# Kernel tuning notes

Hardware: AMD Instinct MI355X
Metric: run time of the kernel (lower is better)

## Reference

```python
import jax, jax.numpy as jnp
import numpy as np

B, N = 4, 8192
NPOINT, NSAMPLE = 2048, 16
IN_PLANES, OUT_PLANES = 64, 128
EPS = 1e-5


def farthest_point_sample(xyz, npoint):
    # xyz: (B, N, 3) -> (B, npoint) int32 indices. Deterministic start at index 0
    # (torch version uses a random start; fixed start keeps the reference reproducible).
    Bb, Nn, _ = xyz.shape

    def step(carry, _):
        distance, farthest = carry                                   # (B,N), (B,)
        centroid = jnp.take_along_axis(xyz, farthest[:, None, None], axis=1)  # (B,1,3)
        dist = jnp.sum((xyz - centroid) ** 2, axis=-1)               # (B,N)
        distance = jnp.minimum(distance, dist)
        new_farthest = jnp.argmax(distance, axis=-1).astype(jnp.int32)
        return (distance, new_farthest), farthest

    init = (jnp.full((Bb, Nn), 1e10, xyz.dtype), jnp.zeros((Bb,), jnp.int32))
    _, cents = jax.lax.scan(step, init, None, length=npoint)         # (npoint, B)
    return cents.T                                                   # (B, npoint)


def setup_inputs() -> dict:
    key = jax.random.key(0)
    k1, k2, k3 = jax.random.split(key, 3)
    px = jax.random.normal(k1, (B, N, IN_PLANES), jnp.float32)
    xyz = jax.random.uniform(k2, (B, N, 3), jnp.float32)
    # Linear(3+in_planes -> out_planes), stored as (in, out)
    W = jax.random.normal(k3, (3 + IN_PLANES, OUT_PLANES), jnp.float32) * 0.1
    b = jnp.zeros((OUT_PLANES,), jnp.float32)
    gamma = jnp.ones((OUT_PLANES,), jnp.float32)
    beta = jnp.zeros((OUT_PLANES,), jnp.float32)
    return {"px": px, "xyz": xyz, "W": W, "b": b, "gamma": gamma, "beta": beta}


def reference(px, xyz, W, b, gamma, beta):
    Bb, Nn, C = px.shape
    cent_idx = farthest_point_sample(xyz, NPOINT)                    # (B, npoint)
    new_xyz = jnp.take_along_axis(xyz, cent_idx[:, :, None], axis=1) # (B, npoint, 3)

    # squared pairwise distances, clamped at 0 (matches square_distance)
    dists = (jnp.sum(new_xyz ** 2, -1)[..., None]
             + jnp.sum(xyz ** 2, -1)[:, None, :]
             - 2.0 * jnp.einsum('bmc,bnc->bmn', new_xyz, xyz))       # (B, npoint, N)
    dists = jnp.maximum(dists, 0.0)

    # KNN: top_k on negated dists == argsort()[:, :, :nsample] up to ties
    _, idx = jax.lax.top_k(-dists, NSAMPLE)                          # (B, npoint, nsample)

    gather = jax.vmap(lambda pts, i: pts[i])                         # per-batch fancy gather
    grouped_xyz = gather(xyz, idx)                                   # (B, npoint, nsample, 3)
    grouped_px = gather(px, idx)                                     # (B, npoint, nsample, C)
    grouped_xyz_norm = grouped_xyz - new_xyz[:, :, None, :]
    grouped = jnp.concatenate([grouped_px, grouped_xyz_norm], axis=-1)

    # Linear -> BatchNorm1d (training-mode batch stats, biased var) -> ReLU
    h = grouped.reshape(-1, C + 3) @ W + b                           # (B*npoint*nsample, out)
    mu = jnp.mean(h, axis=0)
    var = jnp.var(h, axis=0)
    h = (h - mu) / jnp.sqrt(var + EPS) * gamma + beta
    h = jax.nn.relu(h)

    new_px = jnp.max(h.reshape(Bb, NPOINT, NSAMPLE, -1), axis=2)     # (B, npoint, out)
    return new_px, new_xyz
```

## Files before the change

kernel.cpp:

```cpp
#include <hip/hip_runtime.h>
#include <math.h>

#define Bc 4
#define Nc 8192
#define NPOINTc 2048
#define NSAMPLEc 16
#define CINc 64
#define COUTc 128
#define FDIMc 67
#define NBUCK 128
#define EPSc 1e-5f

typedef unsigned long long u64;

__global__ void sq_norm_kernel(const float* __restrict__ xyz, float* __restrict__ sn) {
    int i = blockIdx.x * blockDim.x + threadIdx.x;
    if (i < Bc * Nc) {
        float x = xyz[i * 3], y = xyz[i * 3 + 1], z = xyz[i * 3 + 2];
        sn[i] = __fadd_rn(__fadd_rn(__fmul_rn(x, x), __fmul_rn(y, y)), __fmul_rn(z, z));
    }
}

template <int CTRL>
__device__ __forceinline__ float dpp_maxf(float x) {
    const float o = __int_as_float(__builtin_amdgcn_update_dpp(
        __float_as_int(x), __float_as_int(x), CTRL, 0xF, 0xF, false));
    return fmaxf(x, o);
}
template <int CTRL>
__device__ __forceinline__ unsigned dpp_minu(unsigned x) {
    const unsigned o = (unsigned)__builtin_amdgcn_update_dpp((int)x, (int)x, CTRL, 0xF, 0xF, false);
    return (o < x) ? o : x;
}
template <int CTRL>
__device__ __forceinline__ void kmax_dpp(u64& key) {
    const unsigned lo = (unsigned)key, hi = (unsigned)(key >> 32);
    const unsigned olo = (unsigned)__builtin_amdgcn_update_dpp((int)lo, (int)lo, CTRL, 0xF, 0xF, false);
    const unsigned ohi = (unsigned)__builtin_amdgcn_update_dpp((int)hi, (int)hi, CTRL, 0xF, 0xF, false);
    const u64 okey = ((u64)ohi << 32) | olo;
    key = (okey > key) ? okey : key;
}

__global__ __launch_bounds__(512) void fps_kernel(const float* __restrict__ xyz,
                                                  int* __restrict__ cent,
                                                  float* __restrict__ newxyz) {
    const int b = blockIdx.x;
    const float* base = xyz + (size_t)b * Nc * 3;
    const int t = threadIdx.x;
    const int lane = t & 63, wid = t >> 6;

    __shared__ float P[Nc * 3];
    __shared__ u64   pk[2][8];
    __shared__ int   WIN[NPOINTc];

    for (int e = t; e < Nc * 3; e += 512) P[e] = base[e];

    float X[16], Y[16], Z[16], D[16];
#pragma unroll
    for (int k = 0; k < 16; ++k) {
        const int n = t + (k << 9);
        X[k] = base[n * 3 + 0];
        Y[k] = base[n * 3 + 1];
        Z[k] = base[n * 3 + 2];
        D[k] = 1e10f;
    }
    if (t == 0) WIN[0] = 0;
    __syncthreads();

    float cx = P[0], cy = P[1], cz = P[2];

    for (int it = 1; it < NPOINTc; ++it) {
#pragma unroll
        for (int k = 0; k < 16; ++k) {
            const float dx = __fsub_rn(X[k], cx);
            const float dy = __fsub_rn(Y[k], cy);
            const float dz = __fsub_rn(Z[k], cz);
            const float d2 = __fadd_rn(__fadd_rn(__fmul_rn(dx, dx), __fmul_rn(dy, dy)),
                                       __fmul_rn(dz, dz));
            D[k] = fminf(D[k], d2);
        }
        float a0[8]; int x0[8];
#pragma unroll
        for (int k = 0; k < 8; ++k) {
            const bool g = D[2 * k + 1] > D[2 * k];
            a0[k] = g ? D[2 * k + 1] : D[2 * k];
            x0[k] = t + ((g ? (2 * k + 1) : (2 * k)) << 9);
        }
        float a1[4]; int x1[4];
#pragma unroll
        for (int k = 0; k < 4; ++k) {
            const bool g = a0[2 * k + 1] > a0[2 * k];
            a1[k] = g ? a0[2 * k + 1] : a0[2 * k];
            x1[k] = g ? x0[2 * k + 1] : x0[2 * k];
        }
        float a2[2]; int x2[2];
#pragma unroll
        for (int k = 0; k < 2; ++k) {
            const bool g = a1[2 * k + 1] > a1[2 * k];
            a2[k] = g ? a1[2 * k + 1] : a1[2 * k];
            x2[k] = g ? x1[2 * k + 1] : x1[2 * k];
        }
        const bool gf = a2[1] > a2[0];
        const float bd = gf ? a2[1] : a2[0];
        const int   bi = gf ? x2[1] : x2[0];

        float wv = bd;
        wv = dpp_maxf<0x111>(wv);
        wv = dpp_maxf<0x112>(wv);
        wv = dpp_maxf<0x114>(wv);
        wv = dpp_maxf<0x118>(wv);
        wv = dpp_maxf<0x142>(wv);
        wv = dpp_maxf<0x143>(wv);
        const float v = __int_as_float(__builtin_amdgcn_readlane(__float_as_int(wv), 63));

        unsigned cand = (bd == v) ? (unsigned)bi : 0xffffffffu;
        cand = dpp_minu<0x111>(cand);
        cand = dpp_minu<0x112>(cand);
        cand = dpp_minu<0x114>(cand);
        cand = dpp_minu<0x118>(cand);
        cand = dpp_minu<0x142>(cand);
        cand = dpp_minu<0x143>(cand);

        const int par = it & 1;
        if (lane == 63) pk[par][wid] = ((u64)__float_as_uint(v) << 32) | (unsigned)(~cand);
        __syncthreads();

        u64 k8 = pk[par][lane & 7];
        if (lane >= 8) k8 = 0;
        kmax_dpp<0x111>(k8);
        kmax_dpp<0x112>(k8);
        kmax_dpp<0x114>(k8);
        const unsigned lo7 = (unsigned)__builtin_amdgcn_readlane((int)(unsigned)k8, 7);
        const int riv = (int)~lo7;

        cx = P[riv * 3 + 0]; cy = P[riv * 3 + 1]; cz = P[riv * 3 + 2];
        if (t == 0) WIN[it] = riv;
    }
    __syncthreads();

    for (int e = t; e < NPOINTc; e += 512) {
        const int wv2 = WIN[e];
        cent[b * NPOINTc + e] = wv2;
        float* o = newxyz + ((size_t)b * NPOINTc + e) * 3;
        o[0] = P[wv2 * 3 + 0]; o[1] = P[wv2 * 3 + 1]; o[2] = P[wv2 * 3 + 2];
    }
}

__global__ __launch_bounds__(64) void knn_kernel(const float* __restrict__ xyz,
                                                 const float* __restrict__ sn,
                                                 const int* __restrict__ cent,
                                                 int* __restrict__ knn) {
    const int g = blockIdx.x;
    const int b = g >> 11;
    const int lane = threadIdx.x;
    const float* base = xyz + (size_t)b * Nc * 3;
    const float* snb = sn + (size_t)b * Nc;

    const int cm = cent[g];
    const float mx = base[cm * 3 + 0];
    const float my = base[cm * 3 + 1];
    const float mz = base[cm * 3 + 2];
    const float s1 = snb[cm];

    float dls[16];
    int   ils[16];
#pragma unroll
    for (int j = 0; j < 16; ++j) { dls[j] = INFINITY; ils[j] = -1; }

    for (int jj = 0; jj < Nc / 64; ++jj) {
        const int n = lane + (jj << 6);
        const float x = base[n * 3 + 0];
        const float y = base[n * 3 + 1];
        const float z = base[n * 3 + 2];
        const float dot = fmaf(z, mz, fmaf(y, my, __fmul_rn(x, mx)));
        float d = __fadd_rn(__fadd_rn(__fmul_rn(-2.0f, dot), s1), snb[n]);
        d = fmaxf(d, 0.0f);
        if (d < dls[15]) {
            float cd = d; int ci = n;
#pragma unroll
            for (int j = 0; j < 16; ++j) {
                const bool less = cd < dls[j];
                const float td = less ? dls[j] : cd;
                const int   ti = less ? ils[j] : ci;
                dls[j] = less ? cd : dls[j];
                ils[j] = less ? ci : ils[j];
                cd = td; ci = ti;
            }
        }
    }

    __shared__ float ld[64][16];
    __shared__ int   li[64][16];
#pragma unroll
    for (int j = 0; j < 16; ++j) { ld[lane][j] = dls[j]; li[lane][j] = ils[j]; }

    int ptr = 0;
    int* out = knn + (size_t)g * NSAMPLEc;
    for (int r = 0; r < NSAMPLEc; ++r) {
        const float hd = ld[lane][ptr];
        const int   hi = li[lane][ptr];
        float vd = hd; int vi = hi;
#pragma unroll
        for (int off = 32; off > 0; off >>= 1) {
            const float od = __shfl_xor(vd, off, 64);
            const int   oi = __shfl_xor(vi, off, 64);
            if (od < vd || (od == vd && oi < vi)) { vd = od; vi = oi; }
        }
        if (hd == vd && hi == vi) ptr++;
        if (lane == r) out[r] = vi;
    }
}

__device__ __forceinline__ void stage_featT(
        const float* __restrict__ px, const float* __restrict__ xyz,
        const float* __restrict__ newxyz, const int* __restrict__ knn,
        int g, int b, int t, float (*featT)[20], int* nidx, float* ctr) {
    if (t < 16) nidx[t] = knn[(size_t)g * NSAMPLEc + t];
    if (t < 3)  ctr[t] = newxyz[(size_t)g * 3 + t];
    __syncthreads();
    for (int e = t; e < 16 * FDIMc; e += 128) {
        const int s = e / FDIMc, i = e % FDIMc;
        float v;
        if (i < CINc) v = px[((size_t)b * Nc + nidx[s]) * CINc + i];
        else          v = __fsub_rn(xyz[((size_t)b * Nc + nidx[s]) * 3 + (i - CINc)], ctr[i - CINc]);
        featT[i][s] = v;
    }
    __syncthreads();
}

__device__ __forceinline__ void gemm_body(const float (*featT)[20], const float* __restrict__ W,
                                          float bc, int t, float* acc) {
#pragma unroll
    for (int r = 0; r < 16; ++r) acc[r] = bc;
    for (int i = 0; i < FDIMc; ++i) {
        const float w = W[i * COUTc + t];
        const float4* fr = (const float4*)featT[i];
        const float4 f0 = fr[0], f1 = fr[1], f2 = fr[2], f3 = fr[3];
        acc[0]  = fmaf(f0.x, w, acc[0]);  acc[1]  = fmaf(f0.y, w, acc[1]);
        acc[2]  = fmaf(f0.z, w, acc[2]);  acc[3]  = fmaf(f0.w, w, acc[3]);
        acc[4]  = fmaf(f1.x, w, acc[4]);  acc[5]  = fmaf(f1.y, w, acc[5]);
        acc[6]  = fmaf(f1.z, w, acc[6]);  acc[7]  = fmaf(f1.w, w, acc[7]);
        acc[8]  = fmaf(f2.x, w, acc[8]);  acc[9]  = fmaf(f2.y, w, acc[9]);
        acc[10] = fmaf(f2.z, w, acc[10]); acc[11] = fmaf(f2.w, w, acc[11]);
        acc[12] = fmaf(f3.x, w, acc[12]); acc[13] = fmaf(f3.y, w, acc[13]);
        acc[14] = fmaf(f3.z, w, acc[14]); acc[15] = fmaf(f3.w, w, acc[15]);
    }
}

__global__ __launch_bounds__(128) void gemm_stats_kernel(
        const float* __restrict__ px, const float* __restrict__ xyz,
        const float* __restrict__ newxyz, const int* __restrict__ knn,
        const float* __restrict__ W, const float* __restrict__ bias,
        float* __restrict__ bsum, float* __restrict__ bsq,
        float* __restrict__ hmax, float* __restrict__ hmin) {
    const int g = blockIdx.x;
    const int b = g >> 11;
    const int t = threadIdx.x;

    __shared__ __align__(16) float featT[FDIMc][20];
    __shared__ int nidx[16];
    __shared__ float ctr[3];
    stage_featT(px, xyz, newxyz, knn, g, b, t, featT, nidx, ctr);

    float acc[16];
    gemm_body(featT, W, bias[t], t, acc);

    float s = 0.f, q = 0.f, mx = acc[0], mn = acc[0];
#pragma unroll
    for (int r = 0; r < 16; ++r) { s += acc[r]; q += acc[r] * acc[r]; }
#pragma unroll
    for (int r = 1; r < 16; ++r) { mx = fmaxf(mx, acc[r]); mn = fminf(mn, acc[r]); }
    atomicAdd(&bsum[(g & (NBUCK - 1)) * COUTc + t], s);
    atomicAdd(&bsq [(g & (NBUCK - 1)) * COUTc + t], q);
    if (hmax) { hmax[(size_t)g * COUTc + t] = mx; hmin[(size_t)g * COUTc + t] = mn; }
}

__global__ void stats_finalize_kernel(const float* __restrict__ bsum,
                                      const float* __restrict__ bsq,
                                      const float* __restrict__ gamma,
                                      const float* __restrict__ beta,
                                      float* __restrict__ scsh) {
    const int c = threadIdx.x;
    float S = 0.f, Q = 0.f;
    for (int k = 0; k < NBUCK; ++k) { S += bsum[k * COUTc + c]; Q += bsq[k * COUTc + c]; }
    const float cnt = (float)(Bc * NPOINTc * NSAMPLEc);
    const float mu = S / cnt;
    const float var = Q / cnt - mu * mu;
    const float sc = gamma[c] / sqrtf(var + EPSc);
    scsh[c] = sc;
    scsh[COUTc + c] = beta[c] - mu * sc;
}

__global__ __launch_bounds__(256) void finalize_out_kernel(
        const float* __restrict__ hmax, const float* __restrict__ hmin,
        const float* __restrict__ scsh, float* __restrict__ out) {
    const int i = blockIdx.x * 256 + threadIdx.x;
    const int c = i & (COUTc - 1);
    const float sc = scsh[c], sh = scsh[COUTc + c];
    const float sel = (sc > 0.f) ? hmax[i] : hmin[i];
    out[i] = fmaxf(fmaf(sel, sc, sh), 0.0f);
}

__global__ __launch_bounds__(128) void gemm_out_kernel(
        const float* __restrict__ px, const float* __restrict__ xyz,
        const float* __restrict__ newxyz, const int* __restrict__ knn,
        const float* __restrict__ W, const float* __restrict__ bias,
        const float* __restrict__ scsh, float* __restrict__ out) {
    const int g = blockIdx.x;
    const int b = g >> 11;
    const int t = threadIdx.x;

    __shared__ __align__(16) float featT[FDIMc][20];
    __shared__ int nidx[16];
    __shared__ float ctr[3];
    stage_featT(px, xyz, newxyz, knn, g, b, t, featT, nidx, ctr);

    float acc[16];
    gemm_body(featT, W, bias[t], t, acc);

    const float sc = scsh[t], sh = scsh[COUTc + t];
    float m = -INFINITY;
#pragma unroll
    for (int r = 0; r < 16; ++r) {
        const float v = fmaxf(fmaf(acc[r], sc, sh), 0.0f);
        m = fmaxf(m, v);
    }
    out[(size_t)g * COUTc + t] = m;
}

extern "C" void kernel_launch(void* const* d_in, const int* in_sizes, int n_in,
                              void* d_out, int out_size, void* d_ws, size_t ws_size,
                              hipStream_t stream) {
    const float* px    = (const float*)d_in[0];
    const float* xyz   = (const float*)d_in[1];
    const float* W     = (const float*)d_in[2];
    const float* bias  = (const float*)d_in[3];
    const float* gamma = (const float*)d_in[4];
    const float* beta  = (const float*)d_in[5];

    float* out_px = (float*)d_out;
    float* out_nx = out_px + (size_t)Bc * NPOINTc * COUTc;

    char* w0 = (char*)d_ws;
    char* w = w0;
    int*   cent = (int*)w;    w += (size_t)Bc * NPOINTc * 4;
    float* sn   = (float*)w;  w += (size_t)Bc * Nc * 4;
    int*   knn  = (int*)w;    w += (size_t)Bc * NPOINTc * NSAMPLEc * 4;
    float* bsum = (float*)w;  w += (size_t)NBUCK * COUTc * 4;
    float* bsq  = (float*)w;  w += (size_t)NBUCK * COUTc * 4;
    float* scsh = (float*)w;  w += 2 * COUTc * 4;
    float* hmax = (float*)w;  w += (size_t)Bc * NPOINTc * COUTc * 4;
    float* hmin = (float*)w;  w += (size_t)Bc * NPOINTc * COUTc * 4;
    const bool fused = ((size_t)(w - w0) <= ws_size);

    hipMemsetAsync(bsum, 0, (size_t)NBUCK * COUTc * 4 * 2, stream);

    sq_norm_kernel<<<(Bc * Nc + 255) / 256, 256, 0, stream>>>(xyz, sn);
    fps_kernel<<<Bc, 512, 0, stream>>>(xyz, cent, out_nx);
    knn_kernel<<<Bc * NPOINTc, 64, 0, stream>>>(xyz, sn, cent, knn);
    gemm_stats_kernel<<<Bc * NPOINTc, 128, 0, stream>>>(px, xyz, out_nx, knn, W, bias,
                                                        bsum, bsq,
                                                        fused ? hmax : nullptr,
                                                        fused ? hmin : nullptr);
    stats_finalize_kernel<<<1, 128, 0, stream>>>(bsum, bsq, gamma, beta, scsh);
    if (fused) {
        finalize_out_kernel<<<(Bc * NPOINTc * COUTc) / 256, 256, 0, stream>>>(hmax, hmin, scsh, out_px);
    } else {
        gemm_out_kernel<<<Bc * NPOINTc, 128, 0, stream>>>(px, xyz, out_nx, knn, W, bias, scsh, out_px);
    }
}
```

Before: 2.711 ms.

## Morton-sort FPS points per thread and skip distance updates via bounding-box bound

The FPS kernel now bins points into a 16^3 Morton grid, sorts them with a shared-memory histogram and scan, and gives each thread 16 spatially nearby points along with their bounding box. Each iteration, a thread computes a lower bound on the distance from the new centroid to its box. It skips the distance update and local argmax when that bound cannot lower its current best distance, reusing the cached best value and index. Index tie-breaking is now explicit because the points no longer sit in index order. This adds setup cost, shared memory and per-thread divergence, and in exchange removes most of the per-iteration arithmetic once the centroids spread out.

```diff
diff --git a/kernel.cpp b/kernel.cpp
--- a/kernel.cpp
+++ b/kernel.cpp
@@ -52,58 +52,116 @@
     __shared__ float P[Nc * 3];
     __shared__ u64   pk[2][8];
     __shared__ int   WIN[NPOINTc];
+    __shared__ int   hist[4096];
+    __shared__ int   sidx[Nc];
+    __shared__ int   scanb[512];
 
     for (int e = t; e < Nc * 3; e += 512) P[e] = base[e];
-
-    float X[16], Y[16], Z[16], D[16];
-#pragma unroll
-    for (int k = 0; k < 16; ++k) {
-        const int n = t + (k << 9);
-        X[k] = base[n * 3 + 0];
-        Y[k] = base[n * 3 + 1];
-        Z[k] = base[n * 3 + 2];
-        D[k] = 1e10f;
+    for (int e = t; e < 4096; e += 512) hist[e] = 0;
+    __syncthreads();
+
+    unsigned mc[16];
+#pragma unroll
+    for (int j = 0; j < 16; ++j) {
+        const int n = t * 16 + j;
+        const float x = P[n * 3], y = P[n * 3 + 1], z = P[n * 3 + 2];
+        const unsigned xi = (unsigned)fminf(fmaxf(x * 16.f, 0.f), 15.f);
+        const unsigned yi = (unsigned)fminf(fmaxf(y * 16.f, 0.f), 15.f);
+        const unsigned zi = (unsigned)fminf(fmaxf(z * 16.f, 0.f), 15.f);
+        unsigned c = 0;
+#pragma unroll
+        for (int bb = 0; bb < 4; ++bb)
+            c |= (((xi >> bb) & 1u) << (3 * bb + 2)) | (((yi >> bb) & 1u) << (3 * bb + 1))
+               | (((zi >> bb) & 1u) << (3 * bb));
+        mc[j] = c;
+        atomicAdd(&hist[c], 1);
+    }
+    __syncthreads();
+
+    int loc[8]; int s = 0;
+#pragma unroll
+    for (int j = 0; j < 8; ++j) { loc[j] = s; s += hist[t * 8 + j]; }
+    scanb[t] = s;
+    __syncthreads();
+    for (int off = 1; off < 512; off <<= 1) {
+        const int add = (t >= off) ? scanb[t - off] : 0;
+        __syncthreads();
+        scanb[t] += add;
+        __syncthreads();
+    }
+    const int base_off = scanb[t] - s;
+#pragma unroll
+    for (int j = 0; j < 8; ++j) hist[t * 8 + j] = base_off + loc[j];
+    __syncthreads();
+
+#pragma unroll
+    for (int j = 0; j < 16; ++j) {
+        const int slot = atomicAdd(&hist[mc[j]], 1);
+        sidx[slot] = t * 16 + j;
+    }
+    __syncthreads();
+
+    float X[16], Y[16], Z[16], D[16]; int I[16];
+    float bx0 = 1e30f, bx1 = -1e30f, by0 = 1e30f, by1 = -1e30f, bz0 = 1e30f, bz1 = -1e30f;
+#pragma unroll
+    for (int j = 0; j < 16; ++j) {
+        const int si = sidx[t * 16 + j];
+        I[j] = si;
+        const float x = P[si * 3], y = P[si * 3 + 1], z = P[si * 3 + 2];
+        X[j] = x; Y[j] = y; Z[j] = z; D[j] = 1e10f;
+        bx0 = fminf(bx0, x); bx1 = fmaxf(bx1, x);
+        by0 = fminf(by0, y); by1 = fmaxf(by1, y);
+        bz0 = fminf(bz0, z); bz1 = fmaxf(bz1, z);
     }
     if (t == 0) WIN[0] = 0;
     __syncthreads();
 
     float cx = P[0], cy = P[1], cz = P[2];
+    float bd = 1e10f; int bi = 0x7fffffff;
 
     for (int it = 1; it < NPOINTc; ++it) {
-#pragma unroll
-        for (int k = 0; k < 16; ++k) {
-            const float dx = __fsub_rn(X[k], cx);
-            const float dy = __fsub_rn(Y[k], cy);
-            const float dz = __fsub_rn(Z[k], cz);
-            const float d2 = __fadd_rn(__fadd_rn(__fmul_rn(dx, dx), __fmul_rn(dy, dy)),
-                                       __fmul_rn(dz, dz));
-            D[k] = fminf(D[k], d2);
+        const float gx = fmaxf(0.f, fmaxf(bx0 - cx, cx - bx1));
+        const float gy = fmaxf(0.f, fmaxf(by0 - cy, cy - by1));
+        const float gz = fmaxf(0.f, fmaxf(bz0 - cz, cz - bz1));
+        const float lb = (gx * gx + gy * gy) + gz * gz;
+        if (__fmul_rn(lb, 0.99999f) < bd) {
+#pragma unroll
+            for (int k = 0; k < 16; ++k) {
+                const float dx = __fsub_rn(X[k], cx);
+                const float dy = __fsub_rn(Y[k], cy);
+                const float dz = __fsub_rn(Z[k], cz);
+                const float d2 = __fadd_rn(__fadd_rn(__fmul_rn(dx, dx), __fmul_rn(dy, dy)),
+                                           __fmul_rn(dz, dz));
+                D[k] = fminf(D[k], d2);
+            }
+            float td0[8]; int ti0[8];
+#pragma unroll
+            for (int k = 0; k < 8; ++k) {
+                const bool g = (D[2 * k + 1] > D[2 * k]) ||
+                               (D[2 * k + 1] == D[2 * k] && I[2 * k + 1] < I[2 * k]);
+                td0[k] = g ? D[2 * k + 1] : D[2 * k];
+                ti0[k] = g ? I[2 * k + 1] : I[2 * k];
+            }
+            float td1[4]; int ti1[4];
+#pragma unroll
+            for (int k = 0; k < 4; ++k) {
+                const bool g = (td0[2 * k + 1] > td0[2 * k]) ||
+                               (td0[2 * k + 1] == td0[2 * k] && ti0[2 * k + 1] < ti0[2 * k]);
+                td1[k] = g ? td0[2 * k + 1] : td0[2 * k];
+                ti1[k] = g ? ti0[2 * k + 1] : ti0[2 * k];
+            }
+            float td2[2]; int ti2[2];
+#pragma unroll
+            for (int k = 0; k < 2; ++k) {
+                const bool g = (td1[2 * k + 1] > td1[2 * k]) ||
+                               (td1[2 * k + 1] == td1[2 * k] && ti1[2 * k + 1] < ti1[2 * k]);
+                td2[k] = g ? td1[2 * k + 1] : td1[2 * k];
+                ti2[k] = g ? ti1[2 * k + 1] : ti1[2 * k];
+            }
+            const bool gf = (td2[1] > td2[0]) || (td2[1] == td2[0] && ti2[1] < ti2[0]);
+            bd = gf ? td2[1] : td2[0];
+            bi = gf ? ti2[1] : ti2[0];
         }
-        float a0[8]; int x0[8];
-#pragma unroll
-        for (int k = 0; k < 8; ++k) {
-            const bool g = D[2 * k + 1] > D[2 * k];
-            a0[k] = g ? D[2 * k + 1] : D[2 * k];
-            x0[k] = t + ((g ? (2 * k + 1) : (2 * k)) << 9);
-        }
-        float a1[4]; int x1[4];
-#pragma unroll
-        for (int k = 0; k < 4; ++k) {
-            const bool g = a0[2 * k + 1] > a0[2 * k];
-            a1[k] = g ? a0[2 * k + 1] : a0[2 * k];
-            x1[k] = g ? x0[2 * k + 1] : x0[2 * k];
-        }
-        float a2[2]; int x2[2];
-#pragma unroll
-        for (int k = 0; k < 2; ++k) {
-            const bool g = a1[2 * k + 1] > a1[2 * k];
-            a2[k] = g ? a1[2 * k + 1] : a1[2 * k];
-            x2[k] = g ? x1[2 * k + 1] : x1[2 * k];
-        }
-        const bool gf = a2[1] > a2[0];
-        const float bd = gf ? a2[1] : a2[0];
-        const int   bi = gf ? x2[1] : x2[0];
-
         float wv = bd;
         wv = dpp_maxf<0x111>(wv);
         wv = dpp_maxf<0x112>(wv);
```

Result: slower. 5.628 ms (+107.6%).
